# Kernel optimization log

Measured on AMD Instinct MI355X. Metric: run time of the kernel, lower is better.

Reference implementation:

```python
import jax, jax.numpy as jnp
import numpy as np

H_, W_, KNN, KO = 64, 64, 32, 32
TAU, ETA, LAMBDA0, ALPHA = 1.5, 8.0, 0.001, 10.0
A_, B_, BETA, BETA_P = 1.0, 0.0, 8.0, 8.0
SMOOTH_KS, SMOOTH_SIGMA, EPS = 5, 1.0, 1e-6


def _base_grid(h, w):
    ys = jnp.arange(h, dtype=jnp.float32)
    xs = jnp.arange(w, dtype=jnp.float32)
    yy, xx = jnp.meshgrid(ys, xs, indexing='ij')
    return jnp.stack([xx.reshape(-1), yy.reshape(-1)], axis=-1)  # (N,2) as (x,y)


def _offset_bins(K_o, h, w):
    maxr = (h ** 2 + w ** 2) ** 0.5 * 0.5
    ks = jnp.arange(1, K_o + 1, dtype=jnp.float32)
    angles = 2.0 * jnp.pi * (ks - 1) / K_o
    radii = 0.2 * maxr + 0.6 * maxr * (ks - 1) / (K_o - 1 + 1e-9)
    return jnp.stack([radii * jnp.cos(angles), radii * jnp.sin(angles)], axis=-1)  # (K_o,2)


def _gaussian_kernel(ks, sigma):
    ax = jnp.arange(-(ks // 2), ks // 2 + 1, dtype=jnp.float32)  # matches torch -ks//2+1 .. ks//2 for odd ks
    xx, yy = jnp.meshgrid(ax, ax, indexing='ij')
    k = jnp.exp(-(xx ** 2 + yy ** 2) / (2.0 * sigma ** 2))
    return (k / k.sum()).reshape(1, 1, ks, ks)


def setup_inputs() -> dict:
    key = jax.random.key(0)
    k1, k2 = jax.random.split(key)
    B, N = 2, H_ * W_
    E = jax.random.normal(k1, (B, N, 256), dtype=jnp.float32)
    A0 = jax.random.uniform(k2, (B, N, N), dtype=jnp.float32)
    return {
        'E': E,
        'A0': A0,
        'P': _base_grid(H_, W_),
        'bins': _offset_bins(KO, H_, W_),
        'smooth_kernel': _gaussian_kernel(SMOOTH_KS, SMOOTH_SIGMA),
    }


def reference(E, A0, P, bins, smooth_kernel):
    B, N, _ = A0.shape
    # top-k neighbors per row (sorted descending, like torch.topk)
    topk_vals, topk_idx = jax.lax.top_k(A0, KNN)  # (B,N,k)

    # offset vectors to neighbors
    p_j = P[topk_idx]                              # (B,N,k,2)
    v = p_j - P[None, :, None, :]                  # (B,N,k,2)
    diff = v[..., None, :] - bins[None, None, None, :, :]   # (B,N,k,K_o,2)
    dist2 = (diff ** 2).sum(-1)                    # (B,N,k,K_o)
    kappa = jnp.exp(-dist2 / (2.0 * TAU ** 2 + 1e-12))

    # global bin histogram and softmax weights
    Hbins = (topk_vals[..., None] * kappa).sum(axis=(1, 2))   # (B,K_o)
    Wsoft = jax.nn.softmax(ETA * Hbins, axis=-1)              # (B,K_o)

    R_edges = LAMBDA0 + (Wsoft[:, None, None, :] * kappa).sum(-1)  # (B,N,k)
    tildeA = topk_vals * R_edges
    A1_edges = tildeA / (tildeA.sum(-1, keepdims=True) + EPS)

    # entropy -> backgroundness U
    p = jax.nn.softmax(ALPHA * A1_edges, axis=-1)
    entropy = -(p * jnp.log(p + EPS)).sum(-1)      # (B,N)
    U = jax.nn.sigmoid(-A_ * entropy + B_)
    m = 1.0 - U

    # mask both endpoints of each edge
    m_j = jax.vmap(jnp.take)(m, topk_idx)          # (B,N,k)
    hatA = m[:, :, None] * A1_edges * m_j
    A2_edges = hatA / (hatA.sum(-1, keepdims=True) + EPS)

    # scatter sparse edges back to dense NxN (row indices unique per row)
    b_idx = jnp.arange(B)[:, None, None]
    n_idx = jnp.arange(N)[None, :, None]
    A2_dense = jnp.zeros((B, N, N), A2_edges.dtype).at[b_idx, n_idx, topk_idx].set(A2_edges)
    A2_dense = A2_dense / (A2_dense.sum(-1, keepdims=True) + EPS)

    # directional evidence
    exp_fwd = jnp.exp(BETA * A2_dense)
    exp_rev = jnp.swapaxes(exp_fwd, -1, -2)
    P_dir = exp_fwd / (exp_fwd + exp_rev + EPS)
    eye = jnp.eye(N, dtype=A2_dense.dtype)
    P_dir = P_dir * (1.0 - eye)                    # zero diagonal
    s_ev = (A2_dense * P_dir).sum(-1)
    A2_T = jnp.swapaxes(A2_dense, -1, -2)
    t_ev = (A2_T * (1.0 - jnp.swapaxes(P_dir, -1, -2))).sum(-1)
    pi_src = s_ev / (s_ev + t_ev + EPS)
    pi_tgt = 1.0 - pi_src

    # spatial attention map
    W_mean = Wsoft.mean(0)                         # (K_o,)
    chi = (kappa * W_mean[None, None, None, :]).sum(-1)       # (B,N,k)
    w_local = jax.nn.softmax(BETA_P * A2_edges, axis=-1)
    q = (w_local * chi).sum(-1)                    # (B,N)
    A1_map = q.reshape(B, 1, H_, W_)
    pad = SMOOTH_KS // 2
    smoothed = jax.lax.conv_general_dilated(A1_map, smooth_kernel, (1, 1), [(pad, pad), (pad, pad)])
    A1_map = jax.nn.sigmoid(smoothed)              # (B,1,h,w)

    return (A2_dense, U, pi_src, pi_tgt, A1_map)
```

## Files before the change

### kernel.cpp

```cpp
#include <hip/hip_runtime.h>
#include <math.h>

#define NN 4096
#define KK 32
#define KOb 32
#define BB 2
#define NSLOT 64

constexpr float EPS = 1e-6f;

typedef float nfloat4 __attribute__((ext_vector_type(4)));

#define WS_VALS   0
#define WS_IDX    (WS_VALS + BB*NN*KK)
#define WS_HBP    (WS_IDX + BB*NN*KK)
#define WS_A1     (WS_HBP + BB*NSLOT*KOb)
#define WS_M      (WS_A1 + BB*NN*KK)
#define WS_CHI    (WS_M + BB*NN)
#define WS_A2     (WS_CHI + BB*NN*KK)
#define WS_SEV    (WS_A2 + BB*NN*KK)
#define WS_TEV    (WS_SEV + BB*NN)
#define WS_Q      (WS_TEV + BB*NN)

#define OUT_A2   0
#define OUT_U    ((size_t)BB*NN*NN)
#define OUT_PSRC (OUT_U + BB*NN)
#define OUT_PTGT (OUT_PSRC + BB*NN)
#define OUT_MAP  (OUT_PTGT + BB*NN)

__device__ __forceinline__ unsigned int fkey(float x) {
    unsigned int u = __float_as_uint(x);
    return u ^ ((unsigned int)((int)u >> 31) | 0x80000000u);
}
__device__ __forceinline__ float key2f(unsigned int k) {
    unsigned int u = (k & 0x80000000u) ? (k ^ 0x80000000u) : ~k;
    return __uint_as_float(u);
}

__global__ __launch_bounds__(256) void k_topk(const float* __restrict__ A0,
                                              const float* __restrict__ bins,
                                              float* __restrict__ ws) {
    __shared__ float sbins[2 * KOb];
    __shared__ int   scnt[4];
    __shared__ int   swtot[4];
    __shared__ unsigned long long cand[64];
    __shared__ float selv[KK], seldx[KK], seldy[KK];
    __shared__ float shb[KOb];

    const int t = threadIdx.x;
    const int wv = t >> 6, lane = t & 63;
    const int R = blockIdx.x;
    const int b = R >> 12;
    const int r = R & (NN - 1);

    if (t < 2 * KOb) sbins[t] = bins[t];
    if (t < KOb) shb[t] = 0.f;

    const nfloat4* row4 = (const nfloat4*)(A0 + (size_t)R * NN);
    unsigned int key[16];
    #pragma unroll
    for (int i = 0; i < 4; ++i) {
        const nfloat4 f = __builtin_nontemporal_load(row4 + i * 256 + t);
        key[4 * i + 0] = fkey(f.x);
        key[4 * i + 1] = fkey(f.y);
        key[4 * i + 2] = fkey(f.z);
        key[4 * i + 3] = fkey(f.w);
    }

    unsigned int lo = 0u, hi = 0xFFFFFFFFu;
    int cnt = NN, it = 0;
    while (cnt > 64) {
        unsigned int mid;
        if (it == 0)      mid = 0xBF7E0000u;
        else if (it == 1) mid = 0xBF7C4000u;
        else              mid = lo + ((hi - lo) >> 1);
        if (mid <= lo || mid >= hi) mid = lo + ((hi - lo) >> 1);
        if (mid == lo) break;
        int cl = 0;
        #pragma unroll
        for (int j = 0; j < 16; ++j) cl += (key[j] > mid) ? 1 : 0;
        int c = cl;
        #pragma unroll
        for (int m = 32; m >= 1; m >>= 1) c += __shfl_xor(c, m);
        if (lane == 0) scnt[wv] = c;
        __syncthreads();
        const int ctot = scnt[0] + scnt[1] + scnt[2] + scnt[3];
        __syncthreads();
        if (ctot >= KK) { lo = mid; cnt = ctot; } else hi = mid;
        if (++it > 48) break;
    }

    int cl = 0;
    #pragma unroll
    for (int j = 0; j < 16; ++j) cl += (key[j] > lo) ? 1 : 0;
    int inc = cl;
    #pragma unroll
    for (int m = 1; m < 64; m <<= 1) {
        const int o = __shfl_up(inc, m);
        if (lane >= m) inc += o;
    }
    if (lane == 63) swtot[wv] = inc;
    __syncthreads();
    int off = inc - cl;
    #pragma unroll
    for (int w = 0; w < 4; ++w) if (w < wv) off += swtot[w];
    const int nc0 = swtot[0] + swtot[1] + swtot[2] + swtot[3];
    const int ncand = (nc0 < 64) ? nc0 : 64;

    int slot = off;
    #pragma unroll
    for (int j = 0; j < 16; ++j) {
        if (key[j] > lo && slot < 64) {
            const unsigned int gidx = (unsigned int)((j >> 2) * 1024 + t * 4 + (j & 3));
            cand[slot] = ((unsigned long long)key[j] << 32)
                       | (unsigned long long)(4095u - gidx);
            ++slot;
        }
    }
    __syncthreads();

    if (t < 64) {
        const unsigned long long cd = (t < ncand) ? cand[t] : 0ull;
        int rank = 0;
        #pragma unroll
        for (int i = 0; i < 64; ++i) {
            const unsigned long long o = __shfl(cd, i);
            rank += (o > cd) ? 1 : 0;
        }
        if (t < ncand && rank < KK) {
            const float val = key2f((unsigned int)(cd >> 32));
            const int gidx = 4095 - (int)(cd & 0xFFFull);
            ws[WS_VALS + (size_t)R * KK + rank] = val;
            ((int*)(ws + WS_IDX))[(size_t)R * KK + rank] = gidx;
            selv[rank]  = val;
            seldx[rank] = (float)((gidx & 63) - (r & 63));
            seldy[rank] = (float)((gidx >> 6) - (r >> 6));
        }
    }
    __syncthreads();

    const int e = t >> 3;
    const float v = selv[e], dx0 = seldx[e], dy0 = seldy[e];
    #pragma unroll
    for (int jj = 0; jj < 4; ++jj) {
        const int o = (lane & 7) * 4 + jj;
        const float dx = dx0 - sbins[2 * o], dy = dy0 - sbins[2 * o + 1];
        float contrib = v * __expf(-(dx * dx + dy * dy) * (1.0f / 4.5f));
        contrib += __shfl_xor(contrib, 8);
        contrib += __shfl_xor(contrib, 16);
        contrib += __shfl_xor(contrib, 32);
        if ((lane >> 3) == 0) atomicAdd(&shb[o], contrib);
    }
    __syncthreads();
    if (t < KOb)
        atomicAdd(ws + WS_HBP + b * (NSLOT * KOb) + (R & (NSLOT - 1)) * KOb + t,
                  shb[t]);
}

__global__ __launch_bounds__(256) void k_row1(const float* __restrict__ bins,
                                              float* __restrict__ ws,
                                              float* __restrict__ out_u) {
    __shared__ float  sbins[2 * KOb];
    __shared__ float  sHB[BB * KOb];
    __shared__ float  swsoft[BB * KOb];
    __shared__ float4 stbl[BB * KOb];
    const int t = threadIdx.x;
    if (t < 2 * KOb) sbins[t] = bins[t];
    if (t >= 64 && t < 64 + BB * KOb) sHB[t - 64] = 0.f;
    __syncthreads();

    #pragma unroll
    for (int rep = 0; rep < 2; ++rep) {
        const int task = t + 256 * rep;
        const int bo = task & 63;
        const int sg = task >> 6;
        float ps = 0.f;
        #pragma unroll
        for (int s = 0; s < 8; ++s)
            ps += ws[WS_HBP + (bo >> 5) * (NSLOT * KOb) + (sg * 8 + s) * KOb + (bo & 31)];
        atomicAdd(&sHB[bo], ps);
    }
    __syncthreads();
    if (t < BB * KOb) {
        const float h = 8.0f * sHB[t];
        float mx = h;
        #pragma unroll
        for (int m = 16; m >= 1; m >>= 1) mx = fmaxf(mx, __shfl_xor(mx, m));
        const float e = __expf(h - mx);
        float s = e;
        #pragma unroll
        for (int m = 16; m >= 1; m >>= 1) s += __shfl_xor(s, m);
        swsoft[t] = e / s;
    }
    if (t < BB * KOb) {
        const int o = t & 31;
        const float wm = 0.5f * (swsoft[o] + swsoft[KOb + o]);
        stbl[t] = make_float4(sbins[2 * o], sbins[2 * o + 1], swsoft[t], wm);
    }
    __syncthreads();

    const int wv = t >> 6, lane = t & 63;
    const int half = lane >> 5, k = lane & 31;
    const int R = blockIdx.x * 8 + wv * 2 + half;
    const int b = R >> 12;
    const int r = R & (NN - 1);

    const float val = ws[WS_VALS + (size_t)R * KK + k];
    const int c = ((int*)(ws + WS_IDX))[(size_t)R * KK + k];
    const float dx0 = (float)((c & 63) - (r & 63));
    const float dy0 = (float)((c >> 6) - (r >> 6));
    float racc = 0.f, cacc = 0.f;
    const float4* tb = stbl + (b << 5);
    #pragma unroll
    for (int o = 0; o < KOb; ++o) {
        const float4 cb = tb[o];
        const float dx = dx0 - cb.x, dy = dy0 - cb.y;
        const float kap = __expf(-(dx * dx + dy * dy) * (1.0f / 4.5f));
        racc += cb.z * kap;
        cacc += cb.w * kap;
    }
    const float Redge = 0.001f + racc;
    const float chi = cacc;

    const float tilde = val * Redge;
    float s = tilde;
    #pragma unroll
    for (int m = 16; m >= 1; m >>= 1) s += __shfl_xor(s, m);
    const float a1 = tilde / (s + EPS);

    const float z = 10.f * a1;
    float mz = z;
    #pragma unroll
    for (int m = 16; m >= 1; m >>= 1) mz = fmaxf(mz, __shfl_xor(mz, m));
    const float e = __expf(z - mz);
    float se = e;
    #pragma unroll
    for (int m = 16; m >= 1; m >>= 1) se += __shfl_xor(se, m);
    const float p = e / se;
    const float ent_t = -p * __logf(p + EPS);
    float ent = ent_t;
    #pragma unroll
    for (int m = 16; m >= 1; m >>= 1) ent += __shfl_xor(ent, m);
    const float U = 1.f / (1.f + __expf(ent));

    ws[WS_A1  + (size_t)R * KK + k] = a1;
    ws[WS_CHI + (size_t)R * KK + k] = chi;
    if (k == 0) { out_u[R] = U; ws[WS_M + R] = 1.f - U; }
}

__global__ __launch_bounds__(256) void k_row2d(float* __restrict__ ws,
                                               float* __restrict__ outA2) {
    __shared__ float srow[NN];
    __shared__ float sdv[KK];
    __shared__ int   sidx[KK];
    const int R = blockIdx.x;
    const int b = R >> 12;
    const int t = threadIdx.x;

    const int gid = blockIdx.x * 256 + t;
    if (gid < BB * NN) ws[WS_TEV + gid] = 0.f;

    nfloat4* s4 = (nfloat4*)srow;
    const nfloat4 z4 = {0.f, 0.f, 0.f, 0.f};
    #pragma unroll
    for (int i = 0; i < 4; ++i) s4[t + 256 * i] = z4;

    if (t < 64) {
        const int lane = t;
        const bool act = lane < 32;
        const int k = lane;
        const float mi = ws[WS_M + R];
        float a1 = 0.f; int c = 0; float mj = 0.f;
        if (act) {
            a1 = ws[WS_A1 + (size_t)R * KK + k];
            c = ((int*)(ws + WS_IDX))[(size_t)R * KK + k];
            mj = ws[WS_M + b * NN + c];
        }
        const float hat = act ? mi * a1 * mj : 0.f;
        float S = hat;
        #pragma unroll
        for (int m = 16; m >= 1; m >>= 1) S += __shfl_xor(S, m);
        const float a2e = hat / (S + EPS);
        float S2 = a2e;
        #pragma unroll
        for (int m = 16; m >= 1; m >>= 1) S2 += __shfl_xor(S2, m);
        const float dv = a2e / (S2 + EPS);

        const float z = act ? 8.f * a2e : -1e30f;
        float mz = z;
        #pragma unroll
        for (int m = 16; m >= 1; m >>= 1) mz = fmaxf(mz, __shfl_xor(mz, m));
        const float e = act ? __expf(z - mz) : 0.f;
        float se = e;
        #pragma unroll
        for (int m = 16; m >= 1; m >>= 1) se += __shfl_xor(se, m);
        const float wl = e / se;
        const float chi = act ? ws[WS_CHI + (size_t)R * KK + k] : 0.f;
        float q = act ? wl * chi : 0.f;
        #pragma unroll
        for (int m = 16; m >= 1; m >>= 1) q += __shfl_xor(q, m);
        if (lane == 0) ws[WS_Q + R] = q;

        if (act) {
            ws[WS_A2 + (size_t)R * KK + k] = dv;
            sdv[k] = dv;
            sidx[k] = c;
        }
    }
    __syncthreads();
    if (t < KK) srow[sidx[t]] = sdv[t];
    __syncthreads();
    nfloat4* o4 = (nfloat4*)(outA2 + (size_t)R * NN);
    #pragma unroll
    for (int i = 0; i < 4; ++i)
        __builtin_nontemporal_store(s4[t + 256 * i], o4 + t + 256 * i);
}

__global__ __launch_bounds__(256) void k_dir(float* __restrict__ ws) {
    const int t = threadIdx.x;
    const int wv = t >> 6, lane = t & 63;
    const int half = lane >> 5, k = lane & 31;
    const int R = blockIdx.x * 8 + wv * 2 + half;
    const int b = R >> 12;
    const int r = R & (NN - 1);

    const float a = ws[WS_A2 + (size_t)R * KK + k];
    const int c = ((int*)(ws + WS_IDX))[(size_t)R * KK + k];
    float pdir = 0.f;
    if (c != r) {
        const int4* irow = (const int4*)((const int*)(ws + WS_IDX)
                                         + (size_t)(b * NN + c) * KK);
        int p = -1;
        #pragma unroll
        for (int q = 0; q < 8; ++q) {
            const int4 i4 = irow[q];
            if (i4.x == r) p = q * 4 + 0;
            if (i4.y == r) p = q * 4 + 1;
            if (i4.z == r) p = q * 4 + 2;
            if (i4.w == r) p = q * 4 + 3;
        }
        const float arev = (p >= 0) ? ws[WS_A2 + (size_t)(b * NN + c) * KK + p] : 0.f;
        const float ef = __expf(8.f * a), er = __expf(8.f * arev);
        pdir = ef / (ef + er + EPS);
    }
    float s = a * pdir;
    #pragma unroll
    for (int m = 16; m >= 1; m >>= 1) s += __shfl_xor(s, m);
    if (k == 0) ws[WS_SEV + R] = s;
    atomicAdd(ws + WS_TEV + b * NN + c, a * (1.f - pdir));
}

__global__ void k_tail(const float* __restrict__ ws, const float* __restrict__ kern,
                       float* __restrict__ out_psrc, float* __restrict__ out_ptgt,
                       float* __restrict__ out_map) {
    const int i = blockIdx.x * 256 + threadIdx.x;
    const float s = ws[WS_SEV + i], tv = ws[WS_TEV + i];
    const float ps = s / (s + tv + EPS);
    out_psrc[i] = ps;
    out_ptgt[i] = 1.f - ps;

    const int b = i >> 12;
    const int pix = i & 4095;
    const int y = pix >> 6, x = pix & 63;
    float acc = 0.f;
    #pragma unroll
    for (int ky = 0; ky < 5; ++ky) {
        const int yy = y + ky - 2;
        if (yy < 0 || yy >= 64) continue;
        #pragma unroll
        for (int kx = 0; kx < 5; ++kx) {
            const int xx = x + kx - 2;
            if (xx < 0 || xx >= 64) continue;
            acc += ws[WS_Q + b * 4096 + yy * 64 + xx] * kern[ky * 5 + kx];
        }
    }
    out_map[i] = 1.f / (1.f + __expf(-acc));
}

extern "C" void kernel_launch(void* const* d_in, const int* in_sizes, int n_in,
                              void* d_out, int out_size, void* d_ws, size_t ws_size,
                              hipStream_t stream) {
    const float* A0   = (const float*)d_in[1];
    const float* bins = (const float*)d_in[3];
    const float* kern = (const float*)d_in[4];
    float* out = (float*)d_out;
    float* ws  = (float*)d_ws;

    (void)hipMemsetAsync(ws + WS_HBP, 0, BB * NSLOT * KOb * sizeof(float), stream);

    k_topk <<<BB * NN,       256, 0, stream>>>(A0, bins, ws);
    k_row1 <<<BB * NN / 8,   256, 0, stream>>>(bins, ws, out + OUT_U);
    k_row2d<<<BB * NN,       256, 0, stream>>>(ws, out);
    k_dir  <<<BB * NN / 8,   256, 0, stream>>>(ws);
    k_tail <<<BB * NN / 256, 256, 0, stream>>>(ws, kern,
                                               out + OUT_PSRC, out + OUT_PTGT,
                                               out + OUT_MAP);
}
```

Measured before the change: 288.8 us.

## Move histogram softmax into last-block of topk; double-buffer bisection counters

The global histogram reduction and softmax table, previously recomputed redundantly by every k_row1 block, is now computed once by the last k_topk block using an atomic completion counter, and k_row1 just loads the precomputed table. The bisection loop in top-k double-buffers its per-wave counts to drop one barrier per iteration. k_row2d scatters from registers instead of staging through shared arrays. This adds a threadfence and atomic per block and a serialized tail in the last block.

New measurement: 555.6 us. 92.4% more time.

```diff
diff --git a/kernel.cpp b/kernel.cpp
--- a/kernel.cpp
+++ b/kernel.cpp
@@ -14,7 +14,9 @@
 #define WS_VALS   0
 #define WS_IDX    (WS_VALS + BB*NN*KK)
 #define WS_HBP    (WS_IDX + BB*NN*KK)
-#define WS_A1     (WS_HBP + BB*NSLOT*KOb)
+#define WS_CNT    (WS_HBP + BB*NSLOT*KOb)
+#define WS_TBL    (WS_CNT + 4)
+#define WS_A1     (WS_TBL + BB*KOb*4)
 #define WS_M      (WS_A1 + BB*NN*KK)
 #define WS_CHI    (WS_M + BB*NN)
 #define WS_A2     (WS_CHI + BB*NN*KK)
@@ -41,11 +43,13 @@
                                               const float* __restrict__ bins,
                                               float* __restrict__ ws) {
     __shared__ float sbins[2 * KOb];
-    __shared__ int   scnt[4];
+    __shared__ int   scnt[2][4];
     __shared__ int   swtot[4];
     __shared__ unsigned long long cand[64];
     __shared__ float selv[KK], seldx[KK], seldy[KK];
     __shared__ float shb[KOb];
+    __shared__ float sred[64];
+    __shared__ int   slast;
 
     const int t = threadIdx.x;
     const int wv = t >> 6, lane = t & 63;
@@ -82,10 +86,10 @@
         int c = cl;
         #pragma unroll
         for (int m = 32; m >= 1; m >>= 1) c += __shfl_xor(c, m);
-        if (lane == 0) scnt[wv] = c;
+        const int p = it & 1;
+        if (lane == 0) scnt[p][wv] = c;
         __syncthreads();
-        const int ctot = scnt[0] + scnt[1] + scnt[2] + scnt[3];
-        __syncthreads();
+        const int ctot = scnt[p][0] + scnt[p][1] + scnt[p][2] + scnt[p][3];
         if (ctot >= KK) { lo = mid; cnt = ctot; } else hi = mid;
         if (++it > 48) break;
     }
@@ -155,48 +159,51 @@
     if (t < KOb)
         atomicAdd(ws + WS_HBP + b * (NSLOT * KOb) + (R & (NSLOT - 1)) * KOb + t,
                   shb[t]);
-}
-
-__global__ __launch_bounds__(256) void k_row1(const float* __restrict__ bins,
-                                              float* __restrict__ ws,
+
+    __syncthreads();
+    if (t == 0) {
+        __threadfence();
+        const int old = atomicAdd((int*)(ws + WS_CNT), 1);
+        slast = (old == BB * NN - 1) ? 1 : 0;
+    }
+    __syncthreads();
+    if (slast) {
+        __threadfence();
+        if (t < 64) sred[t] = 0.f;
+        __syncthreads();
+        {
+            const int p = t & 63, g = t >> 6;
+            const int bb = p >> 5, oo = p & 31;
+            const volatile float* hb = ws + WS_HBP + bb * (NSLOT * KOb) + oo;
+            float sum = 0.f;
+            for (int s = g * 16; s < g * 16 + 16; ++s)
+                sum += hb[s * KOb];
+            atomicAdd(&sred[p], sum);
+        }
+        __syncthreads();
+        if (t < 64) {
+            const int oo = t & 31;
+            const float h = 8.0f * sred[t];
+            float mx = h;
+            #pragma unroll
+            for (int m = 16; m >= 1; m >>= 1) mx = fmaxf(mx, __shfl_xor(mx, m));
+            const float e2 = __expf(h - mx);
+            float ss = e2;
+            #pragma unroll
+            for (int m = 16; m >= 1; m >>= 1) ss += __shfl_xor(ss, m);
+            const float wsf = e2 / ss;
+            const float wm = 0.5f * (wsf + __shfl_xor(wsf, 32));
+            ((float4*)(ws + WS_TBL))[t] =
+                make_float4(sbins[2 * oo], sbins[2 * oo + 1], wsf, wm);
+        }
+    }
+}
+
+__global__ __launch_bounds__(256) void k_row1(float* __restrict__ ws,
                                               float* __restrict__ out_u) {
-    __shared__ float  sbins[2 * KOb];
-    __shared__ float  sHB[BB * KOb];
-    __shared__ float  swsoft[BB * KOb];
     __shared__ float4 stbl[BB * KOb];
     const int t = threadIdx.x;
-    if (t < 2 * KOb) sbins[t] = bins[t];
-    if (t >= 64 && t < 64 + BB * KOb) sHB[t - 64] = 0.f;
-    __syncthreads();
-
-    #pragma unroll
-    for (int rep = 0; rep < 2; ++rep) {
-        const int task = t + 256 * rep;
-        const int bo = task & 63;
-        const int sg = task >> 6;
-        float ps = 0.f;
-        #pragma unroll
-        for (int s = 0; s < 8; ++s)
-            ps += ws[WS_HBP + (bo >> 5) * (NSLOT * KOb) + (sg * 8 + s) * KOb + (bo & 31)];
-        atomicAdd(&sHB[bo], ps);
-    }
-    __syncthreads();
-    if (t < BB * KOb) {
-        const float h = 8.0f * sHB[t];
-        float mx = h;
-        #pragma unroll
-        for (int m = 16; m >= 1; m >>= 1) mx = fmaxf(mx, __shfl_xor(mx, m));
-        const float e = __expf(h - mx);
-        float s = e;
-        #pragma unroll
-        for (int m = 16; m >= 1; m >>= 1) s += __shfl_xor(s, m);
-        swsoft[t] = e / s;
-    }
-    if (t < BB * KOb) {
-        const int o = t & 31;
-        const float wm = 0.5f * (swsoft[o] + swsoft[KOb + o]);
-        stbl[t] = make_float4(sbins[2 * o], sbins[2 * o + 1], swsoft[t], wm);
-    }
+    if (t < BB * KOb) stbl[t] = ((const float4*)(ws + WS_TBL))[t];
     __syncthreads();
 
     const int wv = t >> 6, lane = t & 63;
@@ -251,8 +258,6 @@
 __global__ __launch_bounds__(256) void k_row2d(float* __restrict__ ws,
                                                float* __restrict__ outA2) {
     __shared__ float srow[NN];
-    __shared__ float sdv[KK];
-    __shared__ int   sidx[KK];
     const int R = blockIdx.x;
     const int b = R >> 12;
     const int t = threadIdx.x;
@@ -265,6 +270,7 @@
     #pragma unroll
     for (int i = 0; i < 4; ++i) s4[t + 256 * i] = z4;
 
+    float dvr = 0.f; int cr = -1;
     if (t < 64) {
         const int lane = t;
         const bool act = lane < 32;
@@ -303,12 +309,11 @@
 
         if (act) {
             ws[WS_A2 + (size_t)R * KK + k] = dv;
-            sdv[k] = dv;
-            sidx[k] = c;
-        }
-    }
-    __syncthreads();
-    if (t < KK) srow[sidx[t]] = sdv[t];
+            dvr = dv; cr = c;
+        }
+    }
+    __syncthreads();
+    if (cr >= 0) srow[cr] = dvr;
     __syncthreads();
     nfloat4* o4 = (nfloat4*)(outA2 + (size_t)R * NN);
     #pragma unroll
@@ -386,10 +391,10 @@
     float* out = (float*)d_out;
     float* ws  = (float*)d_ws;
 
-    (void)hipMemsetAsync(ws + WS_HBP, 0, BB * NSLOT * KOb * sizeof(float), stream);
+    (void)hipMemsetAsync(ws + WS_HBP, 0, (BB * NSLOT * KOb + 4) * sizeof(float), stream);
 
     k_topk <<<BB * NN,       256, 0, stream>>>(A0, bins, ws);
-    k_row1 <<<BB * NN / 8,   256, 0, stream>>>(bins, ws, out + OUT_U);
+    k_row1 <<<BB * NN / 8,   256, 0, stream>>>(ws, out + OUT_U);
     k_row2d<<<BB * NN,       256, 0, stream>>>(ws, out);
     k_dir  <<<BB * NN / 8,   256, 0, stream>>>(ws);
     k_tail <<<BB * NN / 256, 256, 0, stream>>>(ws, kern,
```
